# Performance work log

Hardware: AMD Instinct MI355X
Metric: run time of the kernel (lower is better)

Reference implementation:

```python
import jax, jax.numpy as jnp
import numpy as np

B, IN, H, OUT = 4096, 1024, 1024, 1024


def setup_inputs() -> dict:
    key = jax.random.key(0)
    ks = jax.random.split(key, 16)
    s_in = 1.0 / np.sqrt(IN)
    s_h = 1.0 / np.sqrt(H)
    d = {}
    d['input_vec'] = jax.random.normal(ks[0], (B, IN), jnp.float32)
    d['hidden_vec'] = jax.random.normal(ks[1], (B, H), jnp.float32)
    d['cell_vec'] = jax.random.normal(ks[2], (B, H), jnp.float32)
    names = ['f', 'i', 'o', 'g']
    for j, n in enumerate(names):
        d['Wx_' + n] = jax.random.uniform(ks[3 + 3 * j], (H, IN), jnp.float32, -s_in, s_in)
        d['bx_' + n] = jax.random.uniform(ks[4 + 3 * j], (H,), jnp.float32, -s_in, s_in)
        d['Wh_' + n] = jax.random.uniform(ks[5 + 3 * j], (H, H), jnp.float32, -s_h, s_h)
    d['W_out'] = jax.random.uniform(ks[15], (OUT, H), jnp.float32, -s_h, s_h)
    d['b_out'] = jax.random.uniform(jax.random.fold_in(key, 99), (OUT,), jnp.float32, -s_h, s_h)
    return d


def reference(input_vec, hidden_vec, cell_vec,
              Wx_f, bx_f, Wh_f,
              Wx_i, bx_i, Wh_i,
              Wx_o, bx_o, Wh_o,
              Wx_g, bx_g, Wh_g,
              W_out, b_out):
    # Fuse the 8 small linears into two GEMMs: [B,IN]x[IN,4H] and [B,H]x[H,4H].
    Wx = jnp.concatenate([Wx_f, Wx_i, Wx_o, Wx_g], axis=0)   # [4H, IN]
    Wh = jnp.concatenate([Wh_f, Wh_i, Wh_o, Wh_g], axis=0)   # [4H, H]
    b = jnp.concatenate([bx_f, bx_i, bx_o, bx_g], axis=0)    # [4H]
    gates = input_vec @ Wx.T + hidden_vec @ Wh.T + b          # [B, 4H]
    f, i, o, g = jnp.split(gates, 4, axis=1)
    f = jax.nn.sigmoid(f)
    i = jax.nn.sigmoid(i)
    o = jax.nn.sigmoid(o)
    g = jnp.tanh(g)
    new_cell = f * cell_vec + i * g
    new_hidden = o * jnp.tanh(new_cell)
    output_vec = new_hidden @ W_out.T + b_out
    return (new_hidden, new_cell, output_vec)
```

## Files before the change

### kernel.cpp

```cpp
#include <hip/hip_runtime.h>
#include <hip/hip_bf16.h>
#include <stdint.h>

#define B_   4096
#define IN_  1024
#define H_   1024
#define OUT_ 1024

typedef __attribute__((ext_vector_type(8)))  short short8;
typedef __attribute__((ext_vector_type(16))) float floatx16;

__device__ static inline void gload_lds16(const void* g, void* l) {
    __builtin_amdgcn_global_load_lds(
        (const __attribute__((address_space(1))) unsigned int*)g,
        (__attribute__((address_space(3))) unsigned int*)l,
        16, 0, 0);
}

__device__ static inline float bfbits2f(unsigned int u) {
    union { unsigned int i; float f; } x; x.i = u << 16; return x.f;
}

__global__ void cvt_xh_kernel(const float* __restrict__ x, const float* __restrict__ h,
                              __hip_bfloat16* __restrict__ out) {
    int idx = blockIdx.x * blockDim.x + threadIdx.x;
    int b  = idx >> 9;
    int c4 = (idx & 511) * 4;
    const float* src = (c4 < IN_) ? (x + (size_t)b * IN_ + c4)
                                  : (h + (size_t)b * H_ + (c4 - IN_));
    float4 v = *(const float4*)src;
    __hip_bfloat16* dst = out + (size_t)b * 2048 + c4;
    dst[0] = __float2bfloat16(v.x);
    dst[1] = __float2bfloat16(v.y);
    dst[2] = __float2bfloat16(v.z);
    dst[3] = __float2bfloat16(v.w);
}

struct Ptrs8 { const float* p[8]; };

__global__ void cvt_w_kernel(Ptrs8 ptrs, __hip_bfloat16* __restrict__ out) {
    int idx = blockIdx.x * blockDim.x + threadIdx.x;
    int n  = idx >> 9;
    int c4 = (idx & 511) * 4;
    int gate = n >> 10;
    int r    = n & 1023;
    const float* src = (c4 < 1024) ? (ptrs.p[2 * gate]     + (size_t)r * 1024 + c4)
                                   : (ptrs.p[2 * gate + 1] + (size_t)r * 1024 + (c4 - 1024));
    float4 v = *(const float4*)src;
    __hip_bfloat16* dst = out + (size_t)n * 2048 + c4;
    dst[0] = __float2bfloat16(v.x);
    dst[1] = __float2bfloat16(v.y);
    dst[2] = __float2bfloat16(v.z);
    dst[3] = __float2bfloat16(v.w);
}

__global__ void cvt_kernel(const float* __restrict__ src, __hip_bfloat16* __restrict__ dst, int n4) {
    int idx = blockIdx.x * blockDim.x + threadIdx.x;
    if (idx >= n4) return;
    float4 v = *(const float4*)(src + (size_t)idx * 4);
    __hip_bfloat16* d = dst + (size_t)idx * 4;
    d[0] = __float2bfloat16(v.x);
    d[1] = __float2bfloat16(v.y);
    d[2] = __float2bfloat16(v.z);
    d[3] = __float2bfloat16(v.w);
}

template<int BM, int BN, int WR, int WC>
__global__ __launch_bounds__(256) void gemm_bt(
    const __hip_bfloat16* __restrict__ A,
    const __hip_bfloat16* __restrict__ Bm,
    float* __restrict__ C,
    __hip_bfloat16* __restrict__ Cb,
    const float* __restrict__ bias,
    int M, int N, int K)
{
    constexpr int BK = 64;
    constexpr int TM = BM / WR;
    constexpr int TN = BN / WC;
    constexpr int AM = TM / 32;
    constexpr int AN = TN / 32;
    constexpr int AISS = BM * BK * 2 / 4096;
    constexpr int BISS = BN * BK * 2 / 4096;

    __shared__ __hip_bfloat16 ldsA[BM * BK];
    __shared__ __hip_bfloat16 ldsB[BN * BK];

    const int tid  = threadIdx.x;
    const int lane = tid & 63;
    const int wv   = tid >> 6;
    const int m0   = blockIdx.y * BM;
    const int n0   = blockIdx.x * BN;

    const int srow   = tid >> 3;
    const int schunk = tid & 7;
    const int scg    = schunk ^ (srow & 7);
    const __hip_bfloat16* Ag = A  + (size_t)(m0 + srow) * K + scg * 8;
    const __hip_bfloat16* Bg = Bm + (size_t)(n0 + srow) * K + scg * 8;
    char* lA = (char*)ldsA + wv * 1024;
    char* lB = (char*)ldsB + wv * 1024;

    const int wrow  = (wv / WC) * TM;
    const int wcol  = (wv % WC) * TN;
    const int fr    = lane & 31;
    const int khalf = lane >> 5;

    floatx16 acc[AM][AN] = {};

    for (int k0 = 0; k0 < K; k0 += BK) {
        #pragma unroll
        for (int s = 0; s < AISS; ++s)
            gload_lds16(Ag + (size_t)(s * 32) * K + k0, lA + s * 4096);
        #pragma unroll
        for (int s = 0; s < BISS; ++s)
            gload_lds16(Bg + (size_t)(s * 32) * K + k0, lB + s * 4096);
        __syncthreads();

        #pragma unroll
        for (int kk = 0; kk < 4; ++kk) {
            const int cg = kk * 2 + khalf;
            short8 af[AM], bf[AN];
            #pragma unroll
            for (int i = 0; i < AM; ++i) {
                const int r = wrow + i * 32 + fr;
                af[i] = *(const short8*)((const char*)ldsA + r * 128 + (cg ^ (r & 7)) * 16);
            }
            #pragma unroll
            for (int j = 0; j < AN; ++j) {
                const int r = wcol + j * 32 + fr;
                bf[j] = *(const short8*)((const char*)ldsB + r * 128 + (cg ^ (r & 7)) * 16);
            }
            #pragma unroll
            for (int i = 0; i < AM; ++i)
                #pragma unroll
                for (int j = 0; j < AN; ++j)
                    acc[i][j] = __builtin_amdgcn_mfma_f32_32x32x16_bf16(af[i], bf[j], acc[i][j], 0, 0, 0);
        }
        __syncthreads();
    }

    #pragma unroll
    for (int i = 0; i < AM; ++i) {
        #pragma unroll
        for (int j = 0; j < AN; ++j) {
            const int col = n0 + wcol + j * 32 + fr;
            #pragma unroll
            for (int reg = 0; reg < 16; ++reg) {
                const int row = m0 + wrow + i * 32 + (reg & 3) + 8 * (reg >> 2) + 4 * khalf;
                const float v = acc[i][j][reg];
                if (Cb) {
                    Cb[(size_t)row * N + col] = __float2bfloat16(v);
                } else {
                    C[(size_t)row * N + col] = v + bias[col];
                }
            }
        }
    }
}

__device__ static inline float sigmoidf_(float x) { return 1.0f / (1.0f + __expf(-x)); }
__device__ static inline float tanhf_(float x)    { return 1.0f - 2.0f / (1.0f + __expf(2.0f * x)); }

__global__ void lstm_gate_kernel(const __hip_bfloat16* __restrict__ gates,
                                 const float* __restrict__ cell,
                                 const float* __restrict__ bxf, const float* __restrict__ bxi,
                                 const float* __restrict__ bxo, const float* __restrict__ bxg,
                                 float* __restrict__ new_hidden, float* __restrict__ new_cell,
                                 __hip_bfloat16* __restrict__ h_bf16) {
    int idx = blockIdx.x * blockDim.x + threadIdx.x;
    int b  = idx >> 8;
    int h4 = (idx & 255) * 4;
    const __hip_bfloat16* gr = gates + (size_t)b * (4 * H_);

    uint2 qf = *(const uint2*)(gr + h4);
    uint2 qi = *(const uint2*)(gr + H_ + h4);
    uint2 qo = *(const uint2*)(gr + 2 * H_ + h4);
    uint2 qg = *(const uint2*)(gr + 3 * H_ + h4);
    float4 cv = *(const float4*)(cell + (size_t)b * H_ + h4);
    float4 bf = *(const float4*)(bxf + h4);
    float4 bi = *(const float4*)(bxi + h4);
    float4 bo = *(const float4*)(bxo + h4);
    float4 bg = *(const float4*)(bxg + h4);

    float gf[4] = { bfbits2f(qf.x & 0xffffu), bfbits2f(qf.x >> 16), bfbits2f(qf.y & 0xffffu), bfbits2f(qf.y >> 16) };
    float gi[4] = { bfbits2f(qi.x & 0xffffu), bfbits2f(qi.x >> 16), bfbits2f(qi.y & 0xffffu), bfbits2f(qi.y >> 16) };
    float go[4] = { bfbits2f(qo.x & 0xffffu), bfbits2f(qo.x >> 16), bfbits2f(qo.y & 0xffffu), bfbits2f(qo.y >> 16) };
    float gg[4] = { bfbits2f(qg.x & 0xffffu), bfbits2f(qg.x >> 16), bfbits2f(qg.y & 0xffffu), bfbits2f(qg.y >> 16) };
    float cvv[4] = { cv.x, cv.y, cv.z, cv.w };
    float bfv[4] = { bf.x, bf.y, bf.z, bf.w };
    float biv[4] = { bi.x, bi.y, bi.z, bi.w };
    float bov[4] = { bo.x, bo.y, bo.z, bo.w };
    float bgv[4] = { bg.x, bg.y, bg.z, bg.w };

    float nh[4], nc[4];
    #pragma unroll
    for (int r = 0; r < 4; ++r) {
        float f = sigmoidf_(gf[r] + bfv[r]);
        float i = sigmoidf_(gi[r] + biv[r]);
        float o = sigmoidf_(go[r] + bov[r]);
        float g = tanhf_(gg[r] + bgv[r]);
        float c = f * cvv[r] + i * g;
        nc[r] = c;
        nh[r] = o * tanhf_(c);
    }
    size_t base = (size_t)b * H_ + h4;
    *(float4*)(new_hidden + base) = make_float4(nh[0], nh[1], nh[2], nh[3]);
    *(float4*)(new_cell   + base) = make_float4(nc[0], nc[1], nc[2], nc[3]);
    __hip_bfloat16* hb = h_bf16 + base;
    hb[0] = __float2bfloat16(nh[0]);
    hb[1] = __float2bfloat16(nh[1]);
    hb[2] = __float2bfloat16(nh[2]);
    hb[3] = __float2bfloat16(nh[3]);
}

extern "C" void kernel_launch(void* const* d_in, const int* in_sizes, int n_in,
                              void* d_out, int out_size, void* d_ws, size_t ws_size,
                              hipStream_t stream) {
    const float* input_vec  = (const float*)d_in[0];
    const float* hidden_vec = (const float*)d_in[1];
    const float* cell_vec   = (const float*)d_in[2];
    const float* Wx_f = (const float*)d_in[3];
    const float* bx_f = (const float*)d_in[4];
    const float* Wh_f = (const float*)d_in[5];
    const float* Wx_i = (const float*)d_in[6];
    const float* bx_i = (const float*)d_in[7];
    const float* Wh_i = (const float*)d_in[8];
    const float* Wx_o = (const float*)d_in[9];
    const float* bx_o = (const float*)d_in[10];
    const float* Wh_o = (const float*)d_in[11];
    const float* Wx_g = (const float*)d_in[12];
    const float* bx_g = (const float*)d_in[13];
    const float* Wh_g = (const float*)d_in[14];
    const float* W_out = (const float*)d_in[15];
    const float* b_out = (const float*)d_in[16];

    char* ws = (char*)d_ws;
    __hip_bfloat16* xh    = (__hip_bfloat16*)(ws);
    __hip_bfloat16* Wc    = (__hip_bfloat16*)(ws + (16ull << 20));
    __hip_bfloat16* Wob   = (__hip_bfloat16*)(ws + (32ull << 20));
    __hip_bfloat16* gates = (__hip_bfloat16*)(ws + (34ull << 20));
    __hip_bfloat16* hb    = (__hip_bfloat16*)(ws + (66ull << 20));

    float* new_hidden = (float*)d_out;
    float* new_cell   = new_hidden + (size_t)B_ * H_;
    float* out_vec    = new_cell + (size_t)B_ * H_;

    cvt_xh_kernel<<<(B_ * 512) / 256, 256, 0, stream>>>(input_vec, hidden_vec, xh);
    Ptrs8 p;
    p.p[0] = Wx_f; p.p[1] = Wh_f; p.p[2] = Wx_i; p.p[3] = Wh_i;
    p.p[4] = Wx_o; p.p[5] = Wh_o; p.p[6] = Wx_g; p.p[7] = Wh_g;
    cvt_w_kernel<<<(4096 * 512) / 256, 256, 0, stream>>>(p, Wc);
    cvt_kernel<<<(1024 * 1024 / 4) / 256, 256, 0, stream>>>(W_out, Wob, 1024 * 1024 / 4);

    gemm_bt<128, 128, 2, 2><<<dim3(4 * H_ / 128, B_ / 128), 256, 0, stream>>>(
        xh, Wc, nullptr, gates, nullptr, B_, 4 * H_, 2048);

    lstm_gate_kernel<<<(B_ * H_ / 4) / 256, 256, 0, stream>>>(
        gates, cell_vec, bx_f, bx_i, bx_o, bx_g, new_hidden, new_cell, hb);

    gemm_bt<128, 64, 4, 1><<<dim3(OUT_ / 64, B_ / 128), 256, 0, stream>>>(
        hb, Wob, out_vec, nullptr, b_out, B_, OUT_, H_);
}
```

Before: 281.5 us.

## Fuse LSTM gate epilogue into gate GEMM with interleaved weight rows

Reorders the concatenated gate weight rows so each 128-wide N tile holds 32 hidden units from each of the four gates. The LSTM nonlinearity and cell update can then run directly in the GEMM epilogue, which removes the bf16 gates buffer round trip and the separate gate kernel. It also merges the three conversion kernels into one launch and adds an XCD-aware block-to-tile mapping. The tradeoffs are a 4x1 warp layout where each wave reloads all of B, and scalar uncoalesced epilogue stores.

```diff
diff --git a/kernel.cpp b/kernel.cpp
--- a/kernel.cpp
+++ b/kernel.cpp
@@ -17,79 +17,74 @@
         16, 0, 0);
 }
 
-__device__ static inline float bfbits2f(unsigned int u) {
-    union { unsigned int i; float f; } x; x.i = u << 16; return x.f;
-}
-
-__global__ void cvt_xh_kernel(const float* __restrict__ x, const float* __restrict__ h,
-                              __hip_bfloat16* __restrict__ out) {
-    int idx = blockIdx.x * blockDim.x + threadIdx.x;
-    int b  = idx >> 9;
-    int c4 = (idx & 511) * 4;
-    const float* src = (c4 < IN_) ? (x + (size_t)b * IN_ + c4)
-                                  : (h + (size_t)b * H_ + (c4 - IN_));
+__device__ static inline float sigmoidf_(float x) { return 1.0f / (1.0f + __expf(-x)); }
+__device__ static inline float tanhf_(float x)    { return 1.0f - 2.0f / (1.0f + __expf(2.0f * x)); }
+
+struct Ptrs8 { const float* p[8]; };
+
+__global__ void cvt_all_kernel(const float* __restrict__ x, const float* __restrict__ h,
+                               Ptrs8 ptrs, const float* __restrict__ wout,
+                               __hip_bfloat16* __restrict__ xh,
+                               __hip_bfloat16* __restrict__ Wc,
+                               __hip_bfloat16* __restrict__ Wob) {
+    int blk = blockIdx.x;
+    const float* src;
+    __hip_bfloat16* dst;
+    if (blk < 8192) {
+        int idx = blk * 256 + threadIdx.x;
+        int b  = idx >> 9;
+        int c4 = (idx & 511) * 4;
+        src = (c4 < IN_) ? (x + (size_t)b * IN_ + c4)
+                         : (h + (size_t)b * H_ + (c4 - IN_));
+        dst = xh + (size_t)b * 2048 + c4;
+    } else if (blk < 16384) {
+        int idx = (blk - 8192) * 256 + threadIdx.x;
+        int n  = idx >> 9;
+        int c4 = (idx & 511) * 4;
+        int gate = (n >> 5) & 3;
+        int hh   = ((n >> 7) << 5) + (n & 31);
+        src = (c4 < 1024) ? (ptrs.p[2 * gate]     + (size_t)hh * 1024 + c4)
+                          : (ptrs.p[2 * gate + 1] + (size_t)hh * 1024 + (c4 - 1024));
+        dst = Wc + (size_t)n * 2048 + c4;
+    } else {
+        int idx = (blk - 16384) * 256 + threadIdx.x;
+        src = wout + (size_t)idx * 4;
+        dst = Wob + (size_t)idx * 4;
+    }
     float4 v = *(const float4*)src;
-    __hip_bfloat16* dst = out + (size_t)b * 2048 + c4;
     dst[0] = __float2bfloat16(v.x);
     dst[1] = __float2bfloat16(v.y);
     dst[2] = __float2bfloat16(v.z);
     dst[3] = __float2bfloat16(v.w);
 }
 
-struct Ptrs8 { const float* p[8]; };
-
-__global__ void cvt_w_kernel(Ptrs8 ptrs, __hip_bfloat16* __restrict__ out) {
-    int idx = blockIdx.x * blockDim.x + threadIdx.x;
-    int n  = idx >> 9;
-    int c4 = (idx & 511) * 4;
-    int gate = n >> 10;
-    int r    = n & 1023;
-    const float* src = (c4 < 1024) ? (ptrs.p[2 * gate]     + (size_t)r * 1024 + c4)
-                                   : (ptrs.p[2 * gate + 1] + (size_t)r * 1024 + (c4 - 1024));
-    float4 v = *(const float4*)src;
-    __hip_bfloat16* dst = out + (size_t)n * 2048 + c4;
-    dst[0] = __float2bfloat16(v.x);
-    dst[1] = __float2bfloat16(v.y);
-    dst[2] = __float2bfloat16(v.z);
-    dst[3] = __float2bfloat16(v.w);
-}
-
-__global__ void cvt_kernel(const float* __restrict__ src, __hip_bfloat16* __restrict__ dst, int n4) {
-    int idx = blockIdx.x * blockDim.x + threadIdx.x;
-    if (idx >= n4) return;
-    float4 v = *(const float4*)(src + (size_t)idx * 4);
-    __hip_bfloat16* d = dst + (size_t)idx * 4;
-    d[0] = __float2bfloat16(v.x);
-    d[1] = __float2bfloat16(v.y);
-    d[2] = __float2bfloat16(v.z);
-    d[3] = __float2bfloat16(v.w);
-}
-
-template<int BM, int BN, int WR, int WC>
-__global__ __launch_bounds__(256) void gemm_bt(
+__global__ __launch_bounds__(256) void gemm_gate_fused(
     const __hip_bfloat16* __restrict__ A,
     const __hip_bfloat16* __restrict__ Bm,
-    float* __restrict__ C,
-    __hip_bfloat16* __restrict__ Cb,
-    const float* __restrict__ bias,
-    int M, int N, int K)
+    const float* __restrict__ cell,
+    const float* __restrict__ bxf, const float* __restrict__ bxi,
+    const float* __restrict__ bxo, const float* __restrict__ bxg,
+    float* __restrict__ new_hidden, float* __restrict__ new_cell,
+    __hip_bfloat16* __restrict__ hb)
 {
     constexpr int BK = 64;
-    constexpr int TM = BM / WR;
-    constexpr int TN = BN / WC;
-    constexpr int AM = TM / 32;
-    constexpr int AN = TN / 32;
-    constexpr int AISS = BM * BK * 2 / 4096;
-    constexpr int BISS = BN * BK * 2 / 4096;
-
-    __shared__ __hip_bfloat16 ldsA[BM * BK];
-    __shared__ __hip_bfloat16 ldsB[BN * BK];
+    constexpr int K  = 2048;
+    constexpr int N  = 4096;
+
+    __shared__ __hip_bfloat16 ldsA[128 * BK];
+    __shared__ __hip_bfloat16 ldsB[128 * BK];
 
     const int tid  = threadIdx.x;
     const int lane = tid & 63;
     const int wv   = tid >> 6;
-    const int m0   = blockIdx.y * BM;
-    const int n0   = blockIdx.x * BN;
+
+    const int bid    = blockIdx.x;
+    const int xcd    = bid & 7;
+    const int loc    = bid >> 3;
+    const int n_tile = xcd * 4 + (loc & 3);
+    const int m_tile = loc >> 2;
+    const int m0 = m_tile * 128;
+    const int n0 = n_tile * 128;
 
     const int srow   = tid >> 3;
     const int schunk = tid & 7;
@@ -99,117 +94,138 @@
     char* lA = (char*)ldsA + wv * 1024;
     char* lB = (char*)ldsB + wv * 1024;
 
-    const int wrow  = (wv / WC) * TM;
-    const int wcol  = (wv % WC) * TN;
+    const int wrow  = wv * 32;
     const int fr    = lane & 31;
     const int khalf = lane >> 5;
 
-    floatx16 acc[AM][AN] = {};
+    floatx16 acc[4] = {};
 
     for (int k0 = 0; k0 < K; k0 += BK) {
         #pragma unroll
-        for (int s = 0; s < AISS; ++s)
+        for (int s = 0; s < 4; ++s)
             gload_lds16(Ag + (size_t)(s * 32) * K + k0, lA + s * 4096);
         #pragma unroll
-        for (int s = 0; s < BISS; ++s)
+        for (int s = 0; s < 4; ++s)
             gload_lds16(Bg + (size_t)(s * 32) * K + k0, lB + s * 4096);
         __syncthreads();
 
         #pragma unroll
         for (int kk = 0; kk < 4; ++kk) {
             const int cg = kk * 2 + khalf;
-            short8 af[AM], bf[AN];
-            #pragma unroll
-            for (int i = 0; i < AM; ++i) {
-                const int r = wrow + i * 32 + fr;
-                af[i] = *(const short8*)((const char*)ldsA + r * 128 + (cg ^ (r & 7)) * 16);
+            const int ra = wrow + fr;
+            short8 af = *(const short8*)((const char*)ldsA + ra * 128 + ((cg ^ (ra & 7)) * 16));
+            short8 bf[4];
+            #pragma unroll
+            for (int j = 0; j < 4; ++j) {
+                const int r = j * 32 + fr;
+                bf[j] = *(const short8*)((const char*)ldsB + r * 128 + ((cg ^ (r & 7)) * 16));
             }
             #pragma unroll
-            for (int j = 0; j < AN; ++j) {
-                const int r = wcol + j * 32 + fr;
-                bf[j] = *(const short8*)((const char*)ldsB + r * 128 + (cg ^ (r & 7)) * 16);
+            for (int j = 0; j < 4; ++j)
+                acc[j] = __builtin_amdgcn_mfma_f32_32x32x16_bf16(af, bf[j], acc[j], 0, 0, 0);
+        }
+        __syncthreads();
+    }
+
+    const int h  = (n0 >> 2) + fr;
+    const float bfb = bxf[h];
+    const float bib = bxi[h];
+    const float bob = bxo[h];
+    const float bgb = bxg[h];
+    const int row_base = m0 + wrow + 4 * khalf;
+
+    #pragma unroll
+    for (int reg = 0; reg < 16; ++reg) {
+        const int row = row_base + (reg & 3) + 8 * (reg >> 2);
+        const size_t off = (size_t)row * H_ + h;
+        const float f = sigmoidf_(acc[0][reg] + bfb);
+        const float i = sigmoidf_(acc[1][reg] + bib);
+        const float o = sigmoidf_(acc[2][reg] + bob);
+        const float g = tanhf_(acc[3][reg] + bgb);
+        const float c = f * cell[off] + i * g;
+        const float nh = o * tanhf_(c);
+        new_cell[off]   = c;
+        new_hidden[off] = nh;
+        hb[off] = __float2bfloat16(nh);
+    }
+}
+
+__global__ __launch_bounds__(256) void gemm_out(
+    const __hip_bfloat16* __restrict__ A,
+    const __hip_bfloat16* __restrict__ Bm,
+    float* __restrict__ C,
+    const float* __restrict__ bias)
+{
+    constexpr int BK = 64;
+    constexpr int K  = 1024;
+    constexpr int N  = 1024;
+
+    __shared__ __hip_bfloat16 ldsA[128 * BK];
+    __shared__ __hip_bfloat16 ldsB[64 * BK];
+
+    const int tid  = threadIdx.x;
+    const int lane = tid & 63;
+    const int wv   = tid >> 6;
+
+    const int bid    = blockIdx.x;
+    const int xcd    = bid & 7;
+    const int loc    = bid >> 3;
+    const int n_tile = xcd * 2 + (loc & 1);
+    const int m_tile = loc >> 1;
+    const int m0 = m_tile * 128;
+    const int n0 = n_tile * 64;
+
+    const int srow   = tid >> 3;
+    const int schunk = tid & 7;
+    const int scg    = schunk ^ (srow & 7);
+    const __hip_bfloat16* Ag = A  + (size_t)(m0 + srow) * K + scg * 8;
+    const __hip_bfloat16* Bg = Bm + (size_t)(n0 + srow) * K + scg * 8;
+    char* lA = (char*)ldsA + wv * 1024;
+    char* lB = (char*)ldsB + wv * 1024;
+
+    const int wrow  = wv * 32;
+    const int fr    = lane & 31;
+    const int khalf = lane >> 5;
+
+    floatx16 acc[2] = {};
+
+    for (int k0 = 0; k0 < K; k0 += BK) {
+        #pragma unroll
+        for (int s = 0; s < 4; ++s)
+            gload_lds16(Ag + (size_t)(s * 32) * K + k0, lA + s * 4096);
+        #pragma unroll
+        for (int s = 0; s < 2; ++s)
+            gload_lds16(Bg + (size_t)(s * 32) * K + k0, lB + s * 4096);
+        __syncthreads();
+
+        #pragma unroll
+        for (int kk = 0; kk < 4; ++kk) {
+            const int cg = kk * 2 + khalf;
+            const int ra = wrow + fr;
+            short8 af = *(const short8*)((const char*)ldsA + ra * 128 + ((cg ^ (ra & 7)) * 16));
+            short8 bf[2];
+            #pragma unroll
+            for (int j = 0; j < 2; ++j) {
+                const int r = j * 32 + fr;
+                bf[j] = *(const short8*)((const char*)ldsB + r * 128 + ((cg ^ (r & 7)) * 16));
             }
             #pragma unroll
-            for (int i = 0; i < AM; ++i)
-                #pragma unroll
-                for (int j = 0; j < AN; ++j)
-                    acc[i][j] = __builtin_amdgcn_mfma_f32_32x32x16_bf16(af[i], bf[j], acc[i][j], 0, 0, 0);
+            for (int j = 0; j < 2; ++j)
+                acc[j] = __builtin_amdgcn_mfma_f32_32x32x16_bf16(af, bf[j], acc[j], 0, 0, 0);
         }
         __syncthreads();
     }
 
     #pragma unroll
-    for (int i = 0; i < AM; ++i) {
-        #pragma unroll
-        for (int j = 0; j < AN; ++j) {
-            const int col = n0 + wcol + j * 32 + fr;
-            #pragma unroll
-            for (int reg = 0; reg < 16; ++reg) {
-                const int row = m0 + wrow + i * 32 + (reg & 3) + 8 * (reg >> 2) + 4 * khalf;
-                const float v = acc[i][j][reg];
-                if (Cb) {
-                    Cb[(size_t)row * N + col] = __float2bfloat16(v);
-                } else {
-                    C[(size_t)row * N + col] = v + bias[col];
-                }
-            }
+    for (int j = 0; j < 2; ++j) {
+        const int col = n0 + j * 32 + fr;
+        const float bb = bias[col];
+        #pragma unroll
+        for (int reg = 0; reg < 16; ++reg) {
+            const int row = m0 + wrow + 4 * khalf + (reg & 3) + 8 * (reg >> 2);
+            C[(size_t)row * N + col] = acc[j][reg] + bb;
         }
     }
-}
-
-__device__ static inline float sigmoidf_(float x) { return 1.0f / (1.0f + __expf(-x)); }
-__device__ static inline float tanhf_(float x)    { return 1.0f - 2.0f / (1.0f + __expf(2.0f * x)); }
-
-__global__ void lstm_gate_kernel(const __hip_bfloat16* __restrict__ gates,
-                                 const float* __restrict__ cell,
-                                 const float* __restrict__ bxf, const float* __restrict__ bxi,
-                                 const float* __restrict__ bxo, const float* __restrict__ bxg,
-                                 float* __restrict__ new_hidden, float* __restrict__ new_cell,
-                                 __hip_bfloat16* __restrict__ h_bf16) {
-    int idx = blockIdx.x * blockDim.x + threadIdx.x;
-    int b  = idx >> 8;
-    int h4 = (idx & 255) * 4;
-    const __hip_bfloat16* gr = gates + (size_t)b * (4 * H_);
-
-    uint2 qf = *(const uint2*)(gr + h4);
-    uint2 qi = *(const uint2*)(gr + H_ + h4);
-    uint2 qo = *(const uint2*)(gr + 2 * H_ + h4);
-    uint2 qg = *(const uint2*)(gr + 3 * H_ + h4);
-    float4 cv = *(const float4*)(cell + (size_t)b * H_ + h4);
-    float4 bf = *(const float4*)(bxf + h4);
-    float4 bi = *(const float4*)(bxi + h4);
-    float4 bo = *(const float4*)(bxo + h4);
-    float4 bg = *(const float4*)(bxg + h4);
-
-    float gf[4] = { bfbits2f(qf.x & 0xffffu), bfbits2f(qf.x >> 16), bfbits2f(qf.y & 0xffffu), bfbits2f(qf.y >> 16) };
-    float gi[4] = { bfbits2f(qi.x & 0xffffu), bfbits2f(qi.x >> 16), bfbits2f(qi.y & 0xffffu), bfbits2f(qi.y >> 16) };
-    float go[4] = { bfbits2f(qo.x & 0xffffu), bfbits2f(qo.x >> 16), bfbits2f(qo.y & 0xffffu), bfbits2f(qo.y >> 16) };
-    float gg[4] = { bfbits2f(qg.x & 0xffffu), bfbits2f(qg.x >> 16), bfbits2f(qg.y & 0xffffu), bfbits2f(qg.y >> 16) };
-    float cvv[4] = { cv.x, cv.y, cv.z, cv.w };
-    float bfv[4] = { bf.x, bf.y, bf.z, bf.w };
-    float biv[4] = { bi.x, bi.y, bi.z, bi.w };
-    float bov[4] = { bo.x, bo.y, bo.z, bo.w };
-    float bgv[4] = { bg.x, bg.y, bg.z, bg.w };
-
-    float nh[4], nc[4];
-    #pragma unroll
-    for (int r = 0; r < 4; ++r) {
-        float f = sigmoidf_(gf[r] + bfv[r]);
-        float i = sigmoidf_(gi[r] + biv[r]);
-        float o = sigmoidf_(go[r] + bov[r]);
-        float g = tanhf_(gg[r] + bgv[r]);
-        float c = f * cvv[r] + i * g;
-        nc[r] = c;
-        nh[r] = o * tanhf_(c);
-    }
-    size_t base = (size_t)b * H_ + h4;
-    *(float4*)(new_hidden + base) = make_float4(nh[0], nh[1], nh[2], nh[3]);
-    *(float4*)(new_cell   + base) = make_float4(nc[0], nc[1], nc[2], nc[3]);
-    __hip_bfloat16* hb = h_bf16 + base;
-    hb[0] = __float2bfloat16(nh[0]);
-    hb[1] = __float2bfloat16(nh[1]);
-    hb[2] = __float2bfloat16(nh[2]);
-    hb[3] = __float2bfloat16(nh[3]);
 }
 
 extern "C" void kernel_launch(void* const* d_in, const int* in_sizes, int n_in,
@@ -234,29 +250,22 @@
     const float* b_out = (const float*)d_in[16];
 
     char* ws = (char*)d_ws;
-    __hip_bfloat16* xh    = (__hip_bfloat16*)(ws);
-    __hip_bfloat16* Wc    = (__hip_bfloat16*)(ws + (16ull << 20));
-    __hip_bfloat16* Wob   = (__hip_bfloat16*)(ws + (32ull << 20));
-    __hip_bfloat16* gates = (__hip_bfloat16*)(ws + (34ull << 20));
-    __hip_bfloat16* hb    = (__hip_bfloat16*)(ws + (66ull << 20));
+    __hip_bfloat16* xh  = (__hip_bfloat16*)(ws);
+    __hip_bfloat16* Wc  = (__hip_bfloat16*)(ws + (16ull << 20));
+    __hip_bfloat16* Wob = (__hip_bfloat16*)(ws + (32ull << 20));
+    __hip_bfloat16* hb  = (__hip_bfloat16*)(ws + (34ull << 20));
 
     float* new_hidden = (float*)d_out;
     float* new_cell   = new_hidden + (size_t)B_ * H_;
     float* out_vec    = new_cell + (size_t)B_ * H_;
 
-    cvt_xh_kernel<<<(B_ * 512) / 256, 256, 0, stream>>>(input_vec, hidden_vec, xh);
     Ptrs8 p;
     p.p[0] = Wx_f; p.p[1] = Wh_f; p.p[2] = Wx_i; p.p[3] = Wh_i;
     p.p[4] = Wx_o; p.p[5] = Wh_o; p.p[6] = Wx_g; p.p[7] = Wh_g;
-    cvt_w_kernel<<<(4096 * 512) / 256, 256, 0, stream>>>(p, Wc);
-    cvt_kernel<<<(1024 * 1024 / 4) / 256, 256, 0, stream>>>(W_out, Wob, 1024 * 1024 / 4);
-
-    gemm_bt<128, 128, 2, 2><<<dim3(4 * H_ / 128, B_ / 128), 256, 0, stream>>>(
-        xh, Wc, nullptr, gates, nullptr, B_, 4 * H_, 2048);
-
-    lstm_gate_kernel<<<(B_ * H_ / 4) / 256, 256, 0, stream>>>(
-        gates, cell_vec, bx_f, bx_i, bx_o, bx_g, new_hidden, new_cell, hb);
-
-    gemm_bt<128, 64, 4, 1><<<dim3(OUT_ / 64, B_ / 128), 256, 0, stream>>>(
-        hb, Wob, out_vec, nullptr, b_out, B_, OUT_, H_);
-}
+    cvt_all_kernel<<<17408, 256, 0, stream>>>(input_vec, hidden_vec, p, W_out, xh, Wc, Wob);
+
+    gemm_gate_fused<<<1024, 256, 0, stream>>>(
+        xh, Wc, cell_vec, bx_f, bx_i, bx_o, bx_g, new_hidden, new_cell, hb);
+
+    gemm_out<<<512, 256, 0, stream>>>(hb, Wob, out_vec, b_out);
+}
```

Measured after the change: 249.0 us. 11.5% less time.
